# Kernel optimization log

Hardware: AMD Instinct MI355X
Metric: run time of the kernel (lower is better)

## Reference

```python
import jax, jax.numpy as jnp
import numpy as np

D = 1024
H = 16
HD = D // H  # head_dim = 64
B, S = 2, 2048


def setup_inputs() -> dict:
    key = jax.random.key(0)
    ks = jax.random.split(key, 5)
    scale = 1.0 / np.sqrt(D)
    return {
        "sequences": jax.random.normal(ks[0], (B, S, D), dtype=jnp.float32),
        "Wq": jax.random.normal(ks[1], (D, D), dtype=jnp.float32) * scale,
        "bq": jnp.zeros((D,), dtype=jnp.float32),
        "Wk": jax.random.normal(ks[2], (D, D), dtype=jnp.float32) * scale,
        "bk": jnp.zeros((D,), dtype=jnp.float32),
        "Wv": jax.random.normal(ks[3], (D, D), dtype=jnp.float32) * scale,
        "bv": jnp.zeros((D,), dtype=jnp.float32),
        "Wo": jax.random.normal(ks[4], (D, D), dtype=jnp.float32) * scale,
        "bo": jnp.zeros((D,), dtype=jnp.float32),
    }


def _split_heads(x):
    # [B, S, D] -> [B, H, S, HD]
    b, s, _ = x.shape
    return x.reshape(b, s, H, HD).transpose(0, 2, 1, 3)


def reference(sequences, Wq, bq, Wk, bk, Wv, bv, Wo, bo):
    b, s, _ = sequences.shape
    q = _split_heads(sequences @ Wq + bq)  # [B,H,S,HD]
    k = _split_heads(sequences @ Wk + bk)
    v = _split_heads(sequences @ Wv + bv)
    inv_sqrt_hd = jnp.asarray(1.0 / np.sqrt(HD), dtype=sequences.dtype)
    scores = jnp.einsum("bhqd,bhkd->bhqk", q, k) * inv_sqrt_hd  # [B,H,S,S]
    attn = jax.nn.softmax(scores, axis=-1)
    ctx = jnp.einsum("bhqk,bhkd->bhqd", attn, v)  # [B,H,S,HD]
    ctx = ctx.transpose(0, 2, 1, 3).reshape(b, s, D)  # merge heads
    return ctx @ Wo + bo
```

## Files before the change

### kernel.cpp

```cpp
#include <hip/hip_runtime.h>
#include <hip/hip_bf16.h>
#include <cstdint>

#define D 1024
#define H 16
#define HD 64
#define B 2
#define S 2048
#define NTOK (B * S)

typedef __bf16 bf16x8 __attribute__((ext_vector_type(8)));
typedef float f32x4 __attribute__((ext_vector_type(4)));

__device__ __forceinline__ unsigned short f2bf(float x) {
  __bf16 b = (__bf16)x;
  return __builtin_bit_cast(unsigned short, b);
}

__device__ __forceinline__ bf16x8 ld16(const unsigned short* p) {
  uint4 u = *reinterpret_cast<const uint4*>(p);
  return __builtin_bit_cast(bf16x8, u);
}

__device__ __forceinline__ void gload_lds16(const unsigned short* g, unsigned short* lds) {
  __builtin_amdgcn_global_load_lds(
      (const __attribute__((address_space(1))) void*)g,
      (__attribute__((address_space(3))) void*)lds, 16, 0, 0);
}

__global__ void k_cvt(const float* __restrict__ x, unsigned short* __restrict__ y, int n4) {
  int i = blockIdx.x * blockDim.x + threadIdx.x;
  if (i >= n4) return;
  float4 v = reinterpret_cast<const float4*>(x)[i];
  ushort4 o;
  o.x = f2bf(v.x); o.y = f2bf(v.y); o.z = f2bf(v.z); o.w = f2bf(v.w);
  reinterpret_cast<ushort4*>(y)[i] = o;
}

__global__ void k_transp(const float* __restrict__ w, unsigned short* __restrict__ wt) {
  __shared__ float t[32][33];
  int tx = threadIdx.x & 31, ty = threadIdx.x >> 5;
  int k0 = blockIdx.x * 32, n0 = blockIdx.y * 32;
#pragma unroll
  for (int i = 0; i < 4; ++i)
    t[ty + 8 * i][tx] = w[(size_t)(k0 + ty + 8 * i) * D + n0 + tx];
  __syncthreads();
#pragma unroll
  for (int i = 0; i < 4; ++i)
    wt[(size_t)(n0 + ty + 8 * i) * D + k0 + tx] = f2bf(t[tx][ty + 8 * i]);
}

__global__ __launch_bounds__(256) void k_gemm_qkv(
    const unsigned short* __restrict__ A,
    const unsigned short* __restrict__ Bt,
    const float* __restrict__ bq, const float* __restrict__ bk, const float* __restrict__ bv,
    unsigned short* __restrict__ Qo, unsigned short* __restrict__ Ko, unsigned short* __restrict__ Vo) {
  constexpr int K = 1024;
  __shared__ __align__(16) unsigned short As[2][128 * 32];
  __shared__ __align__(16) unsigned short Bs[2][128 * 32];
  const int tid = threadIdx.x;
  const int lane = tid & 63;
  const int wave = tid >> 6;
  const int l16 = lane & 15, lg = lane >> 4;
  const int wr = wave >> 1, wc = wave & 1;
  const int m0 = blockIdx.x * 128;
  const int n0 = blockIdx.y * 128;

  const int srow = tid >> 2;
  const int skoff = (tid & 3) * 8;
  const int wbase = wave * 512;

  f32x4 acc[4][4] = {};

  auto stage = [&](int buf, int kt) {
    const unsigned short* ga = A + (size_t)(m0 + srow) * K + kt * 32 + skoff;
    gload_lds16(ga, &As[buf][wbase]);
    gload_lds16(ga + (size_t)64 * K, &As[buf][2048 + wbase]);
    const unsigned short* gb = Bt + (size_t)(n0 + srow) * K + kt * 32 + skoff;
    gload_lds16(gb, &Bs[buf][wbase]);
    gload_lds16(gb + (size_t)64 * K, &Bs[buf][2048 + wbase]);
  };

  stage(0, 0);
  int cur = 0;
  for (int kt = 0; kt < K / 32; ++kt) {
    __syncthreads();
    if (kt + 1 < K / 32) stage(cur ^ 1, kt + 1);
    bf16x8 af[4], bfr[4];
#pragma unroll
    for (int mf = 0; mf < 4; ++mf)
      af[mf] = ld16(&As[cur][(wr * 64 + mf * 16 + l16) * 32 + lg * 8]);
#pragma unroll
    for (int nf = 0; nf < 4; ++nf)
      bfr[nf] = ld16(&Bs[cur][(wc * 64 + nf * 16 + l16) * 32 + lg * 8]);
#pragma unroll
    for (int mf = 0; mf < 4; ++mf)
#pragma unroll
      for (int nf = 0; nf < 4; ++nf)
        acc[mf][nf] = __builtin_amdgcn_mfma_f32_16x16x32_bf16(af[mf], bfr[nf], acc[mf][nf], 0, 0, 0);
    cur ^= 1;
  }

  const int seg = n0 >> 10;
  const float* bp = (seg == 0) ? bq : (seg == 1) ? bk : bv;
  const float osc = 0.18033688011112042f;

#pragma unroll
  for (int mf = 0; mf < 4; ++mf) {
#pragma unroll
    for (int nf = 0; nf < 4; ++nf) {
      const int n = n0 + wc * 64 + nf * 16 + l16;
      const int nl = n & 1023;
      const int h = nl >> 6, hd = nl & 63;
      const int mbase = m0 + wr * 64 + mf * 16 + lg * 4;
      const float bval = bp[nl];
      if (seg == 0) {
#pragma unroll
        for (int r = 0; r < 4; ++r) {
          const int m = mbase + r;
          const int b = m >> 11, s = m & 2047;
          Qo[((size_t)(b * H + h) * S + s) * HD + hd] = f2bf((acc[mf][nf][r] + bval) * osc);
        }
      } else if (seg == 1) {
#pragma unroll
        for (int r = 0; r < 4; ++r) {
          const int m = mbase + r;
          const int b = m >> 11, s = m & 2047;
          const size_t idx = (size_t)(b * H + h) * 131072 + (s >> 6) * 4096 +
                             ((s >> 4) & 3) * 1024 + (hd >> 5) * 512 +
                             ((hd >> 3) & 3) * 128 + (s & 15) * 8 + (hd & 7);
          Ko[idx] = f2bf(acc[mf][nf][r] + bval);
        }
      } else {
        const int b = mbase >> 11, s = mbase & 2047;
        const int d = hd;
        const size_t idx = (size_t)(b * H + h) * 131072 + (s >> 6) * 4096 +
                           (d >> 4) * 1024 + ((s >> 5) & 1) * 512 +
                           ((s >> 3) & 3) * 128 + (d & 15) * 8 + (s & 7);
        ushort4 o;
        o.x = f2bf(acc[mf][nf][0] + bval);
        o.y = f2bf(acc[mf][nf][1] + bval);
        o.z = f2bf(acc[mf][nf][2] + bval);
        o.w = f2bf(acc[mf][nf][3] + bval);
        *reinterpret_cast<ushort4*>(&Vo[idx]) = o;
      }
    }
  }
}

__global__ __launch_bounds__(256) void k_gemm_o(
    const unsigned short* __restrict__ A,
    const unsigned short* __restrict__ Bt,
    const float* __restrict__ bias,
    float* __restrict__ C) {
  constexpr int K = 1024, N = 1024;
  __shared__ __align__(16) unsigned short As[2][64 * 32];
  __shared__ __align__(16) unsigned short Bs[2][128 * 32];
  const int tid = threadIdx.x;
  const int lane = tid & 63;
  const int wave = tid >> 6;
  const int l16 = lane & 15, lg = lane >> 4;
  const int wr = wave >> 1, wc = wave & 1;
  const int m0 = blockIdx.x * 64;
  const int n0 = blockIdx.y * 128;

  const int srow = tid >> 2;
  const int skoff = (tid & 3) * 8;
  const int wbase = wave * 512;

  f32x4 acc[2][4] = {};

  auto stage = [&](int buf, int kt) {
    const unsigned short* ga = A + (size_t)(m0 + srow) * K + kt * 32 + skoff;
    gload_lds16(ga, &As[buf][wbase]);
    const unsigned short* gb = Bt + (size_t)(n0 + srow) * K + kt * 32 + skoff;
    gload_lds16(gb, &Bs[buf][wbase]);
    gload_lds16(gb + (size_t)64 * K, &Bs[buf][2048 + wbase]);
  };

  stage(0, 0);
  int cur = 0;
  for (int kt = 0; kt < K / 32; ++kt) {
    __syncthreads();
    if (kt + 1 < K / 32) stage(cur ^ 1, kt + 1);
    bf16x8 af[2], bfr[4];
#pragma unroll
    for (int mf = 0; mf < 2; ++mf)
      af[mf] = ld16(&As[cur][(wr * 32 + mf * 16 + l16) * 32 + lg * 8]);
#pragma unroll
    for (int nf = 0; nf < 4; ++nf)
      bfr[nf] = ld16(&Bs[cur][(wc * 64 + nf * 16 + l16) * 32 + lg * 8]);
#pragma unroll
    for (int mf = 0; mf < 2; ++mf)
#pragma unroll
      for (int nf = 0; nf < 4; ++nf)
        acc[mf][nf] = __builtin_amdgcn_mfma_f32_16x16x32_bf16(af[mf], bfr[nf], acc[mf][nf], 0, 0, 0);
    cur ^= 1;
  }

#pragma unroll
  for (int mf = 0; mf < 2; ++mf) {
#pragma unroll
    for (int nf = 0; nf < 4; ++nf) {
      const int n = n0 + wc * 64 + nf * 16 + l16;
      const int mbase = m0 + wr * 32 + mf * 16 + lg * 4;
      const float bval = bias[n];
#pragma unroll
      for (int r = 0; r < 4; ++r)
        C[(size_t)(mbase + r) * N + n] = acc[mf][nf][r] + bval;
    }
  }
}

__global__ __launch_bounds__(512, 4) void k_attn(
    const unsigned short* __restrict__ Q,
    const unsigned short* __restrict__ Kimg,
    const unsigned short* __restrict__ Vimg,
    unsigned short* __restrict__ Ctx) {
  const int tid = threadIdx.x;
  const int lane = tid & 63;
  const int wave = tid >> 6;
  const int l16 = lane & 15, lg = lane >> 4;

  const int lin = blockIdx.y * 16 + blockIdx.x;
  const int swz = (lin & 7) * 64 + (lin >> 3);
  const int bh = swz >> 4;
  const int q0 = (swz & 15) * 128 + wave * 16;

  __shared__ __align__(16) unsigned short KtL[2][4096];
  __shared__ __align__(16) unsigned short VtL[2][4096];
  __shared__ __align__(16) unsigned short Pl[8][16][72];

  const unsigned short* Qh = Q + ((size_t)bh * S + q0) * HD;
  const unsigned short* Ksrc = Kimg + (size_t)bh * 131072 + tid * 8;
  const unsigned short* Vsrc = Vimg + (size_t)bh * 131072 + tid * 8;

  const bf16x8 qf0 = ld16(Qh + l16 * HD + lg * 8);
  const bf16x8 qf1 = ld16(Qh + l16 * HD + 32 + lg * 8);

  f32x4 ctx[4] = {};
  float m_run = -1e30f, l_run = 0.f;

  gload_lds16(Ksrc, &KtL[0][tid * 8]);
  gload_lds16(Vsrc, &VtL[0][tid * 8]);
  __syncthreads();

  constexpr int NT = S / 64;
  for (int t = 0; t < NT; ++t) {
    const int cur = t & 1;
    if (t + 1 < NT) {
      gload_lds16(Ksrc + (t + 1) * 4096, &KtL[cur ^ 1][tid * 8]);
      gload_lds16(Vsrc + (t + 1) * 4096, &VtL[cur ^ 1][tid * 8]);
    }

    f32x4 st[4];
#pragma unroll
    for (int ks = 0; ks < 4; ++ks) {
      const bf16x8 a0 = ld16(&KtL[cur][ks * 1024 + lane * 8]);
      const bf16x8 a1 = ld16(&KtL[cur][ks * 1024 + 512 + lane * 8]);
      f32x4 a = {};
      a = __builtin_amdgcn_mfma_f32_16x16x32_bf16(a0, qf0, a, 0, 0, 0);
      a = __builtin_amdgcn_mfma_f32_16x16x32_bf16(a1, qf1, a, 0, 0, 0);
      st[ks] = a;
    }

    float tmax = st[0][0];
#pragma unroll
    for (int ks = 0; ks < 4; ++ks)
#pragma unroll
      for (int r = 0; r < 4; ++r)
        tmax = fmaxf(tmax, st[ks][r]);
    tmax = fmaxf(tmax, __shfl_xor(tmax, 16));
    tmax = fmaxf(tmax, __shfl_xor(tmax, 32));
    if (__any(tmax > m_run)) {
      const float m_new = fmaxf(m_run, tmax);
      const float scale = exp2f(m_run - m_new);
      l_run *= scale;
#pragma unroll
      for (int dt = 0; dt < 4; ++dt) ctx[dt] *= scale;
      m_run = m_new;
    }

    float tsum = 0.f;
#pragma unroll
    for (int ks = 0; ks < 4; ++ks) {
      const float p0 = exp2f(st[ks][0] - m_run);
      const float p1 = exp2f(st[ks][1] - m_run);
      const float p2 = exp2f(st[ks][2] - m_run);
      const float p3 = exp2f(st[ks][3] - m_run);
      tsum += (p0 + p1) + (p2 + p3);
      ushort4 pk;
      pk.x = f2bf(p0); pk.y = f2bf(p1); pk.z = f2bf(p2); pk.w = f2bf(p3);
      *reinterpret_cast<ushort4*>(&Pl[wave][l16][ks * 16 + lg * 4]) = pk;
    }
    tsum += __shfl_xor(tsum, 16);
    tsum += __shfl_xor(tsum, 32);
    l_run += tsum;

#pragma unroll
    for (int kk = 0; kk < 2; ++kk) {
      const bf16x8 pf = ld16(&Pl[wave][l16][kk * 32 + lg * 8]);
      __builtin_amdgcn_s_setprio(1);
#pragma unroll
      for (int dt = 0; dt < 4; ++dt) {
        const bf16x8 v = ld16(&VtL[cur][(dt * 2 + kk) * 512 + lane * 8]);
        ctx[dt] = __builtin_amdgcn_mfma_f32_16x16x32_bf16(v, pf, ctx[dt], 0, 0, 0);
      }
      __builtin_amdgcn_s_setprio(0);
    }
    __syncthreads();
  }

  const int b = bh >> 4, h = bh & 15;
  const float inv_l = 1.0f / l_run;
#pragma unroll
  for (int dt = 0; dt < 4; ++dt) {
    ushort4 o;
    o.x = f2bf(ctx[dt][0] * inv_l);
    o.y = f2bf(ctx[dt][1] * inv_l);
    o.z = f2bf(ctx[dt][2] * inv_l);
    o.w = f2bf(ctx[dt][3] * inv_l);
    const size_t off = ((size_t)(b * S + q0 + l16)) * D + h * HD + dt * 16 + lg * 4;
    *reinterpret_cast<ushort4*>(&Ctx[off]) = o;
  }
}

extern "C" void kernel_launch(void* const* d_in, const int* in_sizes, int n_in,
                              void* d_out, int out_size, void* d_ws, size_t ws_size,
                              hipStream_t stream) {
  const float* x  = (const float*)d_in[0];
  const float* Wq = (const float*)d_in[1];
  const float* bq = (const float*)d_in[2];
  const float* Wk = (const float*)d_in[3];
  const float* bk = (const float*)d_in[4];
  const float* Wv = (const float*)d_in[5];
  const float* bv = (const float*)d_in[6];
  const float* Wo = (const float*)d_in[7];
  const float* bo = (const float*)d_in[8];

  char* ws = (char*)d_ws;
  unsigned short* Xb  = (unsigned short*)(ws);
  unsigned short* Wqt = (unsigned short*)(ws + (8u << 20));
  unsigned short* Wkt = (unsigned short*)(ws + (10u << 20));
  unsigned short* Wvt = (unsigned short*)(ws + (12u << 20));
  unsigned short* Wot = (unsigned short*)(ws + (14u << 20));
  unsigned short* Qb  = (unsigned short*)(ws + (16u << 20));
  unsigned short* Kim = (unsigned short*)(ws + (24u << 20));
  unsigned short* Vim = (unsigned short*)(ws + (32u << 20));
  unsigned short* Cx  = Xb;

  k_cvt<<<4096, 256, 0, stream>>>(x, Xb, NTOK * D / 4);
  dim3 tg(32, 32);
  k_transp<<<tg, 256, 0, stream>>>(Wq, Wqt);
  k_transp<<<tg, 256, 0, stream>>>(Wk, Wkt);
  k_transp<<<tg, 256, 0, stream>>>(Wv, Wvt);
  k_transp<<<tg, 256, 0, stream>>>(Wo, Wot);

  k_gemm_qkv<<<dim3(NTOK / 128, 3 * D / 128), 256, 0, stream>>>(
      Xb, Wqt, bq, bk, bv, Qb, Kim, Vim);

  k_attn<<<dim3(S / 128, B * H), 512, 0, stream>>>(Qb, Kim, Vim, Cx);

  k_gemm_o<<<dim3(NTOK / 64, D / 128), 256, 0, stream>>>(Cx, Wot, bo, (float*)d_out);
}
```

Before: 227.9 us.

## Stage QKV GEMM epilogue through LDS for coalesced stores; merge weight transposes

The QKV GEMM epilogue now writes biased, scaled bf16 results into a padded LDS tile (transposed for V) and then emits 16-byte vectorized stores in the Q, K-interleaved and V-interleaved layouts, instead of scattered 2-byte stores. The four weight-transpose launches are merged into one 3D-grid launch writing contiguous buffers. This targets poor store coalescing and launch overhead, at the cost of extra LDS traffic and two barriers, plus a larger shared allocation that may reduce occupancy.

```diff
diff --git a/kernel.cpp b/kernel.cpp
--- a/kernel.cpp
+++ b/kernel.cpp
@@ -37,8 +37,13 @@
   reinterpret_cast<ushort4*>(y)[i] = o;
 }
 
-__global__ void k_transp(const float* __restrict__ w, unsigned short* __restrict__ wt) {
+__global__ void k_transp4(const float* __restrict__ Wq, const float* __restrict__ Wk,
+                          const float* __restrict__ Wv, const float* __restrict__ Wo,
+                          unsigned short* __restrict__ wt0) {
   __shared__ float t[32][33];
+  const int z = blockIdx.z;
+  const float* w = (z == 0) ? Wq : (z == 1) ? Wk : (z == 2) ? Wv : Wo;
+  unsigned short* wt = wt0 + (size_t)z * (D * D);
   int tx = threadIdx.x & 31, ty = threadIdx.x >> 5;
   int k0 = blockIdx.x * 32, n0 = blockIdx.y * 32;
 #pragma unroll
@@ -56,8 +61,9 @@
     const float* __restrict__ bq, const float* __restrict__ bk, const float* __restrict__ bv,
     unsigned short* __restrict__ Qo, unsigned short* __restrict__ Ko, unsigned short* __restrict__ Vo) {
   constexpr int K = 1024;
-  __shared__ __align__(16) unsigned short As[2][128 * 32];
-  __shared__ __align__(16) unsigned short Bs[2][128 * 32];
+  __shared__ __align__(16) unsigned short SMEM[17408];
+  unsigned short* As0 = SMEM;
+  unsigned short* Bs0 = SMEM + 8192;
   const int tid = threadIdx.x;
   const int lane = tid & 63;
   const int wave = tid >> 6;
@@ -74,11 +80,11 @@
 
   auto stage = [&](int buf, int kt) {
     const unsigned short* ga = A + (size_t)(m0 + srow) * K + kt * 32 + skoff;
-    gload_lds16(ga, &As[buf][wbase]);
-    gload_lds16(ga + (size_t)64 * K, &As[buf][2048 + wbase]);
+    gload_lds16(ga, &As0[buf * 4096 + wbase]);
+    gload_lds16(ga + (size_t)64 * K, &As0[buf * 4096 + 2048 + wbase]);
     const unsigned short* gb = Bt + (size_t)(n0 + srow) * K + kt * 32 + skoff;
-    gload_lds16(gb, &Bs[buf][wbase]);
-    gload_lds16(gb + (size_t)64 * K, &Bs[buf][2048 + wbase]);
+    gload_lds16(gb, &Bs0[buf * 4096 + wbase]);
+    gload_lds16(gb + (size_t)64 * K, &Bs0[buf * 4096 + 2048 + wbase]);
   };
 
   stage(0, 0);
@@ -89,10 +95,10 @@
     bf16x8 af[4], bfr[4];
 #pragma unroll
     for (int mf = 0; mf < 4; ++mf)
-      af[mf] = ld16(&As[cur][(wr * 64 + mf * 16 + l16) * 32 + lg * 8]);
+      af[mf] = ld16(&As0[cur * 4096 + (wr * 64 + mf * 16 + l16) * 32 + lg * 8]);
 #pragma unroll
     for (int nf = 0; nf < 4; ++nf)
-      bfr[nf] = ld16(&Bs[cur][(wc * 64 + nf * 16 + l16) * 32 + lg * 8]);
+      bfr[nf] = ld16(&Bs0[cur * 4096 + (wc * 64 + nf * 16 + l16) * 32 + lg * 8]);
 #pragma unroll
     for (int mf = 0; mf < 4; ++mf)
 #pragma unroll
@@ -105,45 +111,64 @@
   const float* bp = (seg == 0) ? bq : (seg == 1) ? bk : bv;
   const float osc = 0.18033688011112042f;
 
+  __syncthreads();
+  unsigned short* Tl = SMEM;
+
 #pragma unroll
   for (int mf = 0; mf < 4; ++mf) {
 #pragma unroll
     for (int nf = 0; nf < 4; ++nf) {
-      const int n = n0 + wc * 64 + nf * 16 + l16;
-      const int nl = n & 1023;
-      const int h = nl >> 6, hd = nl & 63;
-      const int mbase = m0 + wr * 64 + mf * 16 + lg * 4;
-      const float bval = bp[nl];
-      if (seg == 0) {
-#pragma unroll
-        for (int r = 0; r < 4; ++r) {
-          const int m = mbase + r;
-          const int b = m >> 11, s = m & 2047;
-          Qo[((size_t)(b * H + h) * S + s) * HD + hd] = f2bf((acc[mf][nf][r] + bval) * osc);
-        }
-      } else if (seg == 1) {
-#pragma unroll
-        for (int r = 0; r < 4; ++r) {
-          const int m = mbase + r;
-          const int b = m >> 11, s = m & 2047;
-          const size_t idx = (size_t)(b * H + h) * 131072 + (s >> 6) * 4096 +
-                             ((s >> 4) & 3) * 1024 + (hd >> 5) * 512 +
-                             ((hd >> 3) & 3) * 128 + (s & 15) * 8 + (hd & 7);
-          Ko[idx] = f2bf(acc[mf][nf][r] + bval);
-        }
-      } else {
-        const int b = mbase >> 11, s = mbase & 2047;
-        const int d = hd;
-        const size_t idx = (size_t)(b * H + h) * 131072 + (s >> 6) * 4096 +
-                           (d >> 4) * 1024 + ((s >> 5) & 1) * 512 +
-                           ((s >> 3) & 3) * 128 + (d & 15) * 8 + (s & 7);
-        ushort4 o;
-        o.x = f2bf(acc[mf][nf][0] + bval);
-        o.y = f2bf(acc[mf][nf][1] + bval);
-        o.z = f2bf(acc[mf][nf][2] + bval);
-        o.w = f2bf(acc[mf][nf][3] + bval);
-        *reinterpret_cast<ushort4*>(&Vo[idx]) = o;
+      const int ncol = wc * 64 + nf * 16 + l16;
+      const float bval = bp[(n0 & 1023) + ncol];
+#pragma unroll
+      for (int r = 0; r < 4; ++r) {
+        const int row = wr * 64 + mf * 16 + lg * 4 + r;
+        float v = acc[mf][nf][r] + bval;
+        if (seg == 0) v *= osc;
+        if (seg == 2)
+          Tl[ncol * 136 + row] = f2bf(v);
+        else
+          Tl[row * 136 + ncol] = f2bf(v);
       }
+    }
+  }
+  __syncthreads();
+
+  const int b = m0 >> 11, s0 = m0 & 2047;
+  const int h0 = (n0 & 1023) >> 6;
+  if (seg == 0) {
+#pragma unroll
+    for (int i = 0; i < 8; ++i) {
+      const int L = i * 256 + tid;
+      const int r = L >> 4, cc = L & 15;
+      const int h = cc >> 3, hd0 = (cc & 7) * 8;
+      uint4 v = *reinterpret_cast<const uint4*>(&Tl[r * 136 + cc * 8]);
+      *reinterpret_cast<uint4*>(
+          &Qo[((size_t)(b * H + h0 + h) * S + s0 + r) * HD + hd0]) = v;
+    }
+  } else if (seg == 1) {
+    const int T0 = s0 >> 6;
+#pragma unroll
+    for (int i = 0; i < 8; ++i) {
+      const int L = i * 256 + tid;
+      const int h = L >> 10, tt = (L >> 9) & 1, o = (L & 511) * 8;
+      const int key = tt * 64 + ((o >> 10) << 4) + ((o >> 3) & 15);
+      const int col = h * 64 + (((o >> 9) & 1) << 5) + (((o >> 7) & 3) << 3);
+      uint4 v = *reinterpret_cast<const uint4*>(&Tl[key * 136 + col]);
+      *reinterpret_cast<uint4*>(
+          &Ko[(size_t)(b * H + h0 + h) * 131072 + (size_t)(T0 + tt) * 4096 + o]) = v;
+    }
+  } else {
+    const int T0 = s0 >> 6;
+#pragma unroll
+    for (int i = 0; i < 8; ++i) {
+      const int L = i * 256 + tid;
+      const int h = L >> 10, tt = (L >> 9) & 1, o = (L & 511) * 8;
+      const int d = ((o >> 10) << 4) + ((o >> 3) & 15);
+      const int keyl = tt * 64 + (((o >> 9) & 1) << 5) + (((o >> 7) & 3) << 3);
+      uint4 v = *reinterpret_cast<const uint4*>(&Tl[(h * 64 + d) * 136 + keyl]);
+      *reinterpret_cast<uint4*>(
+          &Vo[(size_t)(b * H + h0 + h) * 131072 + (size_t)(T0 + tt) * 4096 + o]) = v;
     }
   }
 }
@@ -341,8 +366,6 @@
   char* ws = (char*)d_ws;
   unsigned short* Xb  = (unsigned short*)(ws);
   unsigned short* Wqt = (unsigned short*)(ws + (8u << 20));
-  unsigned short* Wkt = (unsigned short*)(ws + (10u << 20));
-  unsigned short* Wvt = (unsigned short*)(ws + (12u << 20));
   unsigned short* Wot = (unsigned short*)(ws + (14u << 20));
   unsigned short* Qb  = (unsigned short*)(ws + (16u << 20));
   unsigned short* Kim = (unsigned short*)(ws + (24u << 20));
@@ -350,11 +373,7 @@
   unsigned short* Cx  = Xb;
 
   k_cvt<<<4096, 256, 0, stream>>>(x, Xb, NTOK * D / 4);
-  dim3 tg(32, 32);
-  k_transp<<<tg, 256, 0, stream>>>(Wq, Wqt);
-  k_transp<<<tg, 256, 0, stream>>>(Wk, Wkt);
-  k_transp<<<tg, 256, 0, stream>>>(Wv, Wvt);
-  k_transp<<<tg, 256, 0, stream>>>(Wo, Wot);
+  k_transp4<<<dim3(32, 32, 4), 256, 0, stream>>>(Wq, Wk, Wv, Wo, Wqt);
 
   k_gemm_qkv<<<dim3(NTOK / 128, 3 * D / 128), 256, 0, stream>>>(
       Xb, Wqt, bq, bk, bv, Qb, Kim, Vim);
```

Result: no change. 223.9 us (-1.7%).
